# Kernel tuning notes

Hardware: AMD Instinct MI355X
Metric: run time of the kernel (lower is better)

The kernel has to match this reference:

```python
import jax, jax.numpy as jnp
import numpy as np

N, D, B, C, T, TOD = 8192, 32, 2, 8, 12, 288
PARAM_SCALE = 0.3  # keep relu+softmax logits well-conditioned (original uses plain randn init)


def setup_inputs() -> dict:
    key = jax.random.key(0)
    k0, k1, k2, k3, k4 = jax.random.split(key, 5)
    return {
        "x": jax.random.normal(k0, (B, C, N, T), dtype=jnp.float32),
        "nodevec1": PARAM_SCALE * jax.random.normal(k1, (N, D), dtype=jnp.float32),
        "nodevec2": PARAM_SCALE * jax.random.normal(k2, (N, D), dtype=jnp.float32),
        "timevec": PARAM_SCALE * jax.random.normal(k3, (TOD, D), dtype=jnp.float32),
        "k": PARAM_SCALE * jax.random.normal(k4, (D, D, D), dtype=jnp.float32),
        "time_ind": 100,
    }


def reference(x, nodevec1, nodevec2, timevec, k, time_ind):
    # Dynamic Tucker-decomposition adjacency (SpatialGraphConv.forward, eval mode -> dropout is identity)
    tv = timevec[time_ind]                             # [D]   time_vec
    core = jnp.einsum('d,def->ef', tv, k)              # [D,D] adp1 (squeezed)
    # adp2/adp3 chain: (nodevec1 @ core) @ nodevec2.T  -> [N,N]
    adp = jnp.einsum('ne,ef->nf', nodevec1, core)      # [N,D]
    adp = jnp.einsum('nf,mf->nm', adp, nodevec2)       # [N,N]
    adp = jax.nn.softmax(jax.nn.relu(adp), axis=-1)    # row-softmax over neighbors
    # NConv: neighbor aggregation  'bcnt,nm->bcmt'
    return jnp.einsum('bcnt,nm->bcmt', x, adp)
```

## Files before the change

kernel.cpp:

```cpp
#include <hip/hip_runtime.h>
#include <hip/hip_bf16.h>


#define NN 8192
#define DD 32
#define TT 12
#define NSPLIT 8
#define CHUNK 1024

typedef __attribute__((ext_vector_type(8))) short bf16x8;
typedef __attribute__((ext_vector_type(4))) float f32x4;
typedef __attribute__((ext_vector_type(4))) unsigned int u32x4;

static __device__ __forceinline__ unsigned short f2bf(float f) {
  unsigned int u = __float_as_uint(f);
  u = (u + 0x7FFFu + ((u >> 16) & 1u)) >> 16;
  return (unsigned short)u;
}

static __device__ __forceinline__ float fexp2(float x) {
#if __has_builtin(__builtin_amdgcn_exp2f)
  return __builtin_amdgcn_exp2f(x);
#else
  return __builtin_exp2f(x);
#endif
}

#define MFMA32(A, B, C) __builtin_amdgcn_mfma_f32_16x16x32_bf16((A), (B), (C), 0, 0, 0)

static __device__ __forceinline__ unsigned int pk_rne(float a, float b) {
  unsigned int ua = __float_as_uint(a);
  unsigned int ub = __float_as_uint(b);
  ua = ua + 0x7FFFu + ((ua >> 16) & 1u);
  ub = ub + 0x7FFFu + ((ub >> 16) & 1u);
  return (ua >> 16) | (ub & 0xFFFF0000u);
}

static __device__ __forceinline__ bf16x8 relu_exp2_pack(f32x4 lo, f32x4 hi) {
  u32x4 t;
  t[0] = pk_rne(fexp2(fmaxf(lo[0], 0.f)), fexp2(fmaxf(lo[1], 0.f)));
  t[1] = pk_rne(fexp2(fmaxf(lo[2], 0.f)), fexp2(fmaxf(lo[3], 0.f)));
  t[2] = pk_rne(fexp2(fmaxf(hi[0], 0.f)), fexp2(fmaxf(hi[1], 0.f)));
  t[3] = pk_rne(fexp2(fmaxf(hi[2], 0.f)), fexp2(fmaxf(hi[3], 0.f)));
  return __builtin_bit_cast(bf16x8, t);
}

__global__ __launch_bounds__(256) void k_prep(const float* __restrict__ nv1,
                                              const float* __restrict__ nv2,
                                              const float* __restrict__ timevec,
                                              const float* __restrict__ kk,
                                              const int* __restrict__ tind,
                                              unsigned short* __restrict__ t1b,
                                              unsigned short* __restrict__ nv2b,
                                              float* __restrict__ sums) {
  __shared__ float cs[1024];
  const int tid = threadIdx.x;
  if (tid < 128) sums[blockIdx.x * 128 + tid] = 0.f;
  const float* tv = timevec + (size_t)tind[0] * DD;
  for (int idx = tid; idx < 1024; idx += 256) {
    float acc = 0.f;
#pragma unroll
    for (int d = 0; d < DD; ++d) acc += tv[d] * kk[d * 1024 + idx];
    cs[idx] = acc;
  }
  __syncthreads();
  const int nbase = blockIdx.x * 128;
  const int f = tid & 31, sub = tid >> 5;
#pragma unroll 4
  for (int it = 0; it < 16; ++it) {
    const int n = nbase + it * 8 + sub;
    const float* nr = nv1 + (size_t)n * DD;
    float acc = 0.f;
#pragma unroll
    for (int e = 0; e < DD; ++e) acc += nr[e] * cs[e * DD + f];
    t1b[(size_t)n * DD + f] = f2bf(acc * 1.4426950408889634f);
  }
#pragma unroll 4
  for (int it = 0; it < 16; ++it) {
    const int idx = nbase * DD + it * 256 + tid;
    nv2b[idx] = f2bf(nv2[idx]);
  }
}

__global__ __launch_bounds__(256) void k_stats(const unsigned short* __restrict__ t1b,
                                               const unsigned short* __restrict__ nv2b,
                                               float* __restrict__ sums) {
  const int tid = threadIdx.x;
  const int w = tid >> 6, lane = tid & 63, q = lane >> 4, i16 = lane & 15;
  const int nbase = blockIdx.x * 64 + w * 16;
  bf16x8 a = *(const bf16x8*)(t1b + (size_t)(nbase + i16) * DD + q * 8);
  const f32x4 z4 = {0.f, 0.f, 0.f, 0.f};
  float s[4] = {0.f, 0.f, 0.f, 0.f};
  const int m0 = blockIdx.y * 1024;
  for (int mt = m0; mt < m0 + 1024; mt += 64) {
#pragma unroll
    for (int u = 0; u < 4; ++u) {
      bf16x8 b = *(const bf16x8*)(nv2b + (size_t)(mt + u * 16 + i16) * DD + q * 8);
      f32x4 d = __builtin_amdgcn_mfma_f32_16x16x32_bf16(a, b, z4, 0, 0, 0);
#pragma unroll
      for (int r = 0; r < 4; ++r) s[r] += fexp2(fmaxf(d[r], 0.f));
    }
  }
#pragma unroll
  for (int r = 0; r < 4; ++r)
    for (int off = 1; off < 16; off <<= 1) s[r] += __shfl_xor(s[r], off, 64);
  if (i16 == 0) {
#pragma unroll
    for (int r = 0; r < 4; ++r) atomicAdd(&sums[nbase + q * 4 + r], s[r]);
  }
}

__global__ __launch_bounds__(256) void k_y(const float* __restrict__ x,
                                           const float* __restrict__ sums,
                                           unsigned short* __restrict__ yT) {
  __shared__ float xs[3328];
  const int tid = threadIdx.x;
  const int n0 = blockIdx.x * 256;
  const int bc = blockIdx.y;
  const float* xp = x + (size_t)bc * NN * TT + (size_t)n0 * TT;
#pragma unroll
  for (int j = 0; j < 12; ++j) {
    const int idx = j * 256 + tid;
    xs[(idx / 12) * 13 + idx % 12] = xp[idx];
  }
  __syncthreads();
  const float rinv = 1.0f / sums[n0 + tid];
#pragma unroll
  for (int t = 0; t < 12; ++t)
    yT[(size_t)(bc * TT + t) * NN + n0 + tid] = f2bf(xs[tid * 13 + t] * rinv);
}

__global__ __launch_bounds__(256, 2) void k_mega(const unsigned short* __restrict__ t1b,
                                                 const unsigned short* __restrict__ nv2b,
                                                 const unsigned short* __restrict__ yT,
                                                 float* __restrict__ part) {
  const int tid = threadIdx.x;
  const int w = tid >> 6, lane = tid & 63, q = lane >> 4, i16 = lane & 15;
  const int mw = blockIdx.x * 128 + w * 32;
  const int nt0 = blockIdx.y * CHUNK;

  bf16x8 bg[2];
#pragma unroll
  for (int ms = 0; ms < 2; ++ms)
    bg[ms] = *(const bf16x8*)(nv2b + (size_t)(mw + ms * 16 + i16) * DD + q * 8);

  f32x4 acc[12][2];
#pragma unroll
  for (int c = 0; c < 12; ++c)
#pragma unroll
    for (int ms = 0; ms < 2; ++ms) acc[c][ms] = (f32x4){0.f, 0.f, 0.f, 0.f};

  const int perm = ((i16 >> 2) << 3) | (i16 & 3);
  const unsigned short* tcur = t1b + (size_t)(nt0 + perm) * DD + q * 8;
  int yoff = i16 * NN + nt0 + q * 8;

  const f32x4 z4 = {0.f, 0.f, 0.f, 0.f};

  bf16x8 alo = *(const bf16x8*)tcur;
  bf16x8 ahi = *(const bf16x8*)(tcur + 4 * DD);

  for (int it = 0; it < 32; ++it) {
    bf16x8 y[12];
#pragma unroll
    for (int c = 0; c < 12; ++c)
      y[c] = *(const bf16x8*)(yT + (size_t)(c * 16) * NN + yoff);

    const unsigned short* tnext = tcur + 32 * DD;
    bf16x8 alo_n = *(const bf16x8*)tnext;
    bf16x8 ahi_n = *(const bf16x8*)(tnext + 4 * DD);

    f32x4 d00 = MFMA32(alo, bg[0], z4);
    f32x4 d01 = MFMA32(ahi, bg[0], z4);
    f32x4 d10 = MFMA32(alo, bg[1], z4);
    f32x4 d11 = MFMA32(ahi, bg[1], z4);

    bf16x8 e0 = relu_exp2_pack(d00, d01);
#pragma unroll
    for (int c = 0; c < 12; ++c) acc[c][0] = MFMA32(y[c], e0, acc[c][0]);
    bf16x8 e1 = relu_exp2_pack(d10, d11);
#pragma unroll
    for (int c = 0; c < 12; ++c) acc[c][1] = MFMA32(y[c], e1, acc[c][1]);

    alo = alo_n; ahi = ahi_n;
    tcur = tnext;
    yoff += 32;
  }

  float* pp = part + (size_t)blockIdx.y * 192 * NN;
#pragma unroll
  for (int c = 0; c < 12; ++c)
#pragma unroll
    for (int ms = 0; ms < 2; ++ms) {
      const int colbase = c * 16 + q * 4;
      const int m = mw + ms * 16 + i16;
#pragma unroll
      for (int r = 0; r < 4; ++r)
        pp[(size_t)(colbase + r) * NN + m] = acc[c][ms][r];
    }
}

__global__ __launch_bounds__(256) void k_reduce(const float* __restrict__ part,
                                                float* __restrict__ out) {
  __shared__ float os[3328];
  const int tid = threadIdx.x;
  const int m0 = blockIdx.x * 256;
  const int bc = blockIdx.y;
#pragma unroll
  for (int t = 0; t < 12; ++t) {
    const int col = bc * TT + t;
    float s = 0.f;
#pragma unroll
    for (int nc = 0; nc < NSPLIT; ++nc)
      s += part[((size_t)nc * 192 + col) * NN + m0 + tid];
    os[tid * 13 + t] = s;
  }
  __syncthreads();
  float* op = out + (size_t)bc * NN * TT + (size_t)m0 * TT;
#pragma unroll
  for (int j = 0; j < 12; ++j) {
    const int idx = j * 256 + tid;
    op[idx] = os[(idx / 12) * 13 + idx % 12];
  }
}

extern "C" void kernel_launch(void* const* d_in, const int* in_sizes, int n_in,
                              void* d_out, int out_size, void* d_ws, size_t ws_size,
                              hipStream_t stream) {
  const float* x = (const float*)d_in[0];
  const float* nv1 = (const float*)d_in[1];
  const float* nv2 = (const float*)d_in[2];
  const float* tv = (const float*)d_in[3];
  const float* kk = (const float*)d_in[4];
  const int* tind = (const int*)d_in[5];
  float* out = (float*)d_out;

  char* ws = (char*)d_ws;
  unsigned short* t1b  = (unsigned short*)(ws);
  unsigned short* nv2b = (unsigned short*)(ws + 524288);
  float* sums          = (float*)(ws + 1048576);
  unsigned short* yT   = (unsigned short*)(ws + 1081344);
  float* part          = (float*)(ws + 4227072);

  k_prep<<<64, 256, 0, stream>>>(nv1, nv2, tv, kk, tind, t1b, nv2b, sums);
  k_stats<<<dim3(128, 8), 256, 0, stream>>>(t1b, nv2b, sums);
  k_y<<<dim3(32, 16), 256, 0, stream>>>(x, sums, yT);
  k_mega<<<dim3(64, NSPLIT), 256, 0, stream>>>(t1b, nv2b, yT, part);
  k_reduce<<<dim3(32, 16), 256, 0, stream>>>(part, out);
}
```

Baseline: 210.5 us.

## Split k_mega column work across waves and software-pipeline exp with MFMA

Each wave now handles half of the 192 output columns (6 instead of 12 column tiles) for 32 rows, so a block covers 64 rows and the grid doubles to 128 blocks in x. The score MFMAs and exp packing for the next slice are overlapped with the accumulation MFMAs of the current slice, with y loads prefetched one iteration ahead. Launch bounds are raised to 3 blocks per SIMD. The goal is better occupancy and latency hiding. The cost is recomputing the score/exp tile twice per row block, once in each column-half wave, which duplicates that work.

```diff
diff --git a/kernel.cpp b/kernel.cpp
--- a/kernel.cpp
+++ b/kernel.cpp
@@ -130,13 +130,15 @@
     yT[(size_t)(bc * TT + t) * NN + n0 + tid] = f2bf(xs[tid * 13 + t] * rinv);
 }
 
-__global__ __launch_bounds__(256, 2) void k_mega(const unsigned short* __restrict__ t1b,
+__global__ __launch_bounds__(256, 3) void k_mega(const unsigned short* __restrict__ t1b,
                                                  const unsigned short* __restrict__ nv2b,
                                                  const unsigned short* __restrict__ yT,
                                                  float* __restrict__ part) {
   const int tid = threadIdx.x;
   const int w = tid >> 6, lane = tid & 63, q = lane >> 4, i16 = lane & 15;
-  const int mw = blockIdx.x * 128 + w * 32;
+  const int wm = w >> 1, wc = w & 1;
+  const int mw = blockIdx.x * 64 + wm * 32;
+  const int cw = wc * 96;
   const int nt0 = blockIdx.y * CHUNK;
 
   bf16x8 bg[2];
@@ -144,54 +146,73 @@
   for (int ms = 0; ms < 2; ++ms)
     bg[ms] = *(const bf16x8*)(nv2b + (size_t)(mw + ms * 16 + i16) * DD + q * 8);
 
-  f32x4 acc[12][2];
-#pragma unroll
-  for (int c = 0; c < 12; ++c)
+  f32x4 acc[6][2];
+#pragma unroll
+  for (int c = 0; c < 6; ++c)
 #pragma unroll
     for (int ms = 0; ms < 2; ++ms) acc[c][ms] = (f32x4){0.f, 0.f, 0.f, 0.f};
 
   const int perm = ((i16 >> 2) << 3) | (i16 & 3);
-  const unsigned short* tcur = t1b + (size_t)(nt0 + perm) * DD + q * 8;
-  int yoff = i16 * NN + nt0 + q * 8;
+  const unsigned short* tp = t1b + (size_t)(nt0 + perm) * DD + q * 8;
+  const unsigned short* yp = yT + (size_t)(cw + i16) * NN + nt0 + q * 8;
 
   const f32x4 z4 = {0.f, 0.f, 0.f, 0.f};
 
-  bf16x8 alo = *(const bf16x8*)tcur;
-  bf16x8 ahi = *(const bf16x8*)(tcur + 4 * DD);
-
-  for (int it = 0; it < 32; ++it) {
-    bf16x8 y[12];
-#pragma unroll
-    for (int c = 0; c < 12; ++c)
-      y[c] = *(const bf16x8*)(yT + (size_t)(c * 16) * NN + yoff);
-
-    const unsigned short* tnext = tcur + 32 * DD;
-    bf16x8 alo_n = *(const bf16x8*)tnext;
-    bf16x8 ahi_n = *(const bf16x8*)(tnext + 4 * DD);
-
+  bf16x8 alo = *(const bf16x8*)tp;
+  bf16x8 ahi = *(const bf16x8*)(tp + 4 * DD);
+  bf16x8 e0, e1;
+  {
     f32x4 d00 = MFMA32(alo, bg[0], z4);
     f32x4 d01 = MFMA32(ahi, bg[0], z4);
     f32x4 d10 = MFMA32(alo, bg[1], z4);
     f32x4 d11 = MFMA32(ahi, bg[1], z4);
-
-    bf16x8 e0 = relu_exp2_pack(d00, d01);
-#pragma unroll
-    for (int c = 0; c < 12; ++c) acc[c][0] = MFMA32(y[c], e0, acc[c][0]);
-    bf16x8 e1 = relu_exp2_pack(d10, d11);
-#pragma unroll
-    for (int c = 0; c < 12; ++c) acc[c][1] = MFMA32(y[c], e1, acc[c][1]);
-
+    e0 = relu_exp2_pack(d00, d01);
+    e1 = relu_exp2_pack(d10, d11);
+  }
+  bf16x8 y[6];
+#pragma unroll
+  for (int c = 0; c < 6; ++c) y[c] = *(const bf16x8*)(yp + (size_t)(c * 16) * NN);
+  alo = *(const bf16x8*)(tp + 32 * DD);
+  ahi = *(const bf16x8*)(tp + 36 * DD);
+
+  for (int sl = 1; sl < 32; ++sl) {
+    const int o = sl * 32;
+    bf16x8 yn[6];
+#pragma unroll
+    for (int c = 0; c < 6; ++c)
+      yn[c] = *(const bf16x8*)(yp + (size_t)(c * 16) * NN + o);
+    bf16x8 alo_n = *(const bf16x8*)(tp + (size_t)(o + 32) * DD);
+    bf16x8 ahi_n = *(const bf16x8*)(tp + (size_t)(o + 36) * DD);
+
+    f32x4 d00 = MFMA32(alo, bg[0], z4);
+    f32x4 d01 = MFMA32(ahi, bg[0], z4);
+    f32x4 d10 = MFMA32(alo, bg[1], z4);
+    f32x4 d11 = MFMA32(ahi, bg[1], z4);
+
+#pragma unroll
+    for (int c = 0; c < 6; ++c) acc[c][0] = MFMA32(y[c], e0, acc[c][0]);
+    e0 = relu_exp2_pack(d00, d01);
+#pragma unroll
+    for (int c = 0; c < 6; ++c) acc[c][1] = MFMA32(y[c], e1, acc[c][1]);
+    e1 = relu_exp2_pack(d10, d11);
+
+#pragma unroll
+    for (int c = 0; c < 6; ++c) y[c] = yn[c];
     alo = alo_n; ahi = ahi_n;
-    tcur = tnext;
-    yoff += 32;
+  }
+
+#pragma unroll
+  for (int c = 0; c < 6; ++c) {
+    acc[c][0] = MFMA32(y[c], e0, acc[c][0]);
+    acc[c][1] = MFMA32(y[c], e1, acc[c][1]);
   }
 
   float* pp = part + (size_t)blockIdx.y * 192 * NN;
 #pragma unroll
-  for (int c = 0; c < 12; ++c)
+  for (int c = 0; c < 6; ++c)
 #pragma unroll
     for (int ms = 0; ms < 2; ++ms) {
-      const int colbase = c * 16 + q * 4;
+      const int colbase = cw + c * 16 + q * 4;
       const int m = mw + ms * 16 + i16;
 #pragma unroll
       for (int r = 0; r < 4; ++r)
@@ -244,6 +265,6 @@
   k_prep<<<64, 256, 0, stream>>>(nv1, nv2, tv, kk, tind, t1b, nv2b, sums);
   k_stats<<<dim3(128, 8), 256, 0, stream>>>(t1b, nv2b, sums);
   k_y<<<dim3(32, 16), 256, 0, stream>>>(x, sums, yT);
-  k_mega<<<dim3(64, NSPLIT), 256, 0, stream>>>(t1b, nv2b, yT, part);
+  k_mega<<<dim3(128, NSPLIT), 256, 0, stream>>>(t1b, nv2b, yT, part);
   k_reduce<<<dim3(32, 16), 256, 0, stream>>>(part, out);
 }
```

Result: slower. 218.3 us (+3.7%).
